# Performance work log

Measured on AMD Instinct MI355X. Metric: run time of the kernel, lower is better.

The kernel has to match this reference:

```python
import jax, jax.numpy as jnp
import numpy as np

N_NODES = 100000
NUM_GRAPHS = 128
HEADS = 4
NEG_SLOPE = 0.2  # PyG GATConv default


def _gat_conv(x, src, dst, W, att_s, att_d, bias, heads, n_nodes, concat):
    # x: [N, F_in]; W: [F_in, heads*C]; att_s/att_d: [heads, C]; bias: [heads*C] or [C]
    h = (x @ W).reshape(n_nodes, heads, -1)            # [N, H, C]
    a_s = jnp.einsum('nhc,hc->nh', h, att_s)            # [N, H]
    a_d = jnp.einsum('nhc,hc->nh', h, att_d)            # [N, H]
    e = jax.nn.leaky_relu(a_s[src] + a_d[dst], NEG_SLOPE)  # [E, H]
    m = jax.ops.segment_max(e, dst, num_segments=n_nodes)  # [N, H]
    ex = jnp.exp(e - m[dst])                                # [E, H]
    denom = jax.ops.segment_sum(ex, dst, num_segments=n_nodes)  # [N, H]
    alpha = ex / (denom[dst] + 1e-16)                       # [E, H]
    msg = h[src] * alpha[:, :, None]                        # [E, H, C]
    out = jax.ops.segment_sum(msg, dst, num_segments=n_nodes)  # [N, H, C]
    if concat:
        out = out.reshape(n_nodes, -1)                      # [N, H*C]
    else:
        out = out.mean(axis=1)                              # [N, C]
    return out + bias


def setup_inputs() -> dict:
    key = jax.random.key(0)
    ks = jax.random.split(key, 12)
    in_c, hid, out_c, H = 128, 32, 10, HEADS
    E = 1600000
    x = jax.random.normal(ks[0], (N_NODES, in_c), dtype=jnp.float32)
    edge_index = jax.random.randint(ks[1], (2, E), 0, N_NODES, dtype=jnp.int32)
    batch = jnp.sort(jax.random.randint(ks[2], (N_NODES,), 0, NUM_GRAPHS, dtype=jnp.int32))
    s1 = 1.0 / np.sqrt(in_c)
    s2 = 1.0 / np.sqrt(hid * H)
    W1 = jax.random.uniform(ks[3], (in_c, H * hid), jnp.float32, -s1, s1)
    att_src1 = jax.random.uniform(ks[4], (H, hid), jnp.float32, -s1, s1)
    att_dst1 = jax.random.uniform(ks[5], (H, hid), jnp.float32, -s1, s1)
    b1 = jnp.zeros((H * hid,), jnp.float32)
    W2 = jax.random.uniform(ks[6], (H * hid, out_c), jnp.float32, -s2, s2)
    att_src2 = jax.random.uniform(ks[7], (1, out_c), jnp.float32, -s2, s2)
    att_dst2 = jax.random.uniform(ks[8], (1, out_c), jnp.float32, -s2, s2)
    b2 = jnp.zeros((out_c,), jnp.float32)
    return {"x": x, "W1": W1, "att_src1": att_src1, "att_dst1": att_dst1, "b1": b1,
            "W2": W2, "att_src2": att_src2, "att_dst2": att_dst2, "b2": b2,
            "edge_index": edge_index, "batch": batch}


def reference(x, W1, att_src1, att_dst1, b1, W2, att_src2, att_dst2, b2, edge_index, batch):
    n = x.shape[0]
    loops = jnp.arange(n, dtype=edge_index.dtype)
    src = jnp.concatenate([edge_index[0], loops])  # add_self_loops=True
    dst = jnp.concatenate([edge_index[1], loops])
    h = jax.nn.elu(_gat_conv(x, src, dst, W1, att_src1, att_dst1, b1, HEADS, n, concat=True))
    h = jax.nn.elu(_gat_conv(h, src, dst, W2, att_src2, att_dst2, b2, 1, n, concat=False))
    # global mean pool over graphs
    sums = jax.ops.segment_sum(h, batch, num_segments=NUM_GRAPHS)
    cnts = jax.ops.segment_sum(jnp.ones((n,), h.dtype), batch, num_segments=NUM_GRAPHS)
    pooled = sums / jnp.maximum(cnts, 1.0)[:, None]
    return jax.nn.log_softmax(pooled, axis=1)
```

## Files before the change

### kernel.cpp

```cpp
#include <hip/hip_runtime.h>
#include <cstdint>
#include <cstddef>

#define LRELU(x) fmaxf((x), 0.2f*(x))

typedef float v2f __attribute__((ext_vector_type(2)));
typedef __attribute__((ext_vector_type(8))) short short8;
typedef __attribute__((ext_vector_type(4))) float f32x4;

__device__ inline unsigned short f2bf(float f) {
  unsigned u = __float_as_uint(f);
  u += 0x8000u;
  return (unsigned short)(u >> 16);
}
__device__ inline float bflo(unsigned u) { return __uint_as_float(u << 16); }
__device__ inline float bfhi(unsigned u) { return __uint_as_float(u & 0xffff0000u); }

__global__ __launch_bounds__(256) void k_gemm1(const float* __restrict__ x,
                                               const float* __restrict__ W1,
                                               const float* __restrict__ atts1,
                                               const float* __restrict__ attd1,
                                               int* __restrict__ h1f8,
                                               float* __restrict__ a_s, float* __restrict__ a_d,
                                               int* __restrict__ bcnt,
                                               float* __restrict__ poolcnt,
                                               int N) {
  __shared__ short Wt[128*136];
  int t = threadIdx.x;
  int gid = blockIdx.x*256 + t;
  if (gid < 64) bcnt[gid] = 0;
  if (gid < 1408) poolcnt[gid] = 0.f;

  {
    int n = t & 127, half = t >> 7;
    for (int kk0 = 0; kk0 < 64; kk0 += 4) {
      short v0 = (short)f2bf(W1[(half*64 + kk0 + 0)*128 + n]);
      short v1 = (short)f2bf(W1[(half*64 + kk0 + 1)*128 + n]);
      short v2 = (short)f2bf(W1[(half*64 + kk0 + 2)*128 + n]);
      short v3 = (short)f2bf(W1[(half*64 + kk0 + 3)*128 + n]);
      *(short4*)(&Wt[n*136 + half*64 + kk0]) = make_short4(v0, v1, v2, v3);
    }
  }
  __syncthreads();

  int w = t >> 6, l = t & 63;
  int n0 = blockIdx.x*64 + w*16;
  int mrow = l & 15, q = l >> 4;
  int nrow = n0 + mrow; if (nrow >= N) nrow = N - 1;
  const float4* xrow = (const float4*)(x + (size_t)nrow*128);
  f32x4 acc[8];
  #pragma unroll
  for (int i = 0; i < 8; ++i) acc[i] = (f32x4){0.f, 0.f, 0.f, 0.f};
  #pragma unroll
  for (int kc = 0; kc < 4; ++kc) {
    float4 xa = xrow[kc*8 + q*2];
    float4 xb = xrow[kc*8 + q*2 + 1];
    short8 afr;
    afr[0] = (short)f2bf(xa.x); afr[1] = (short)f2bf(xa.y);
    afr[2] = (short)f2bf(xa.z); afr[3] = (short)f2bf(xa.w);
    afr[4] = (short)f2bf(xb.x); afr[5] = (short)f2bf(xb.y);
    afr[6] = (short)f2bf(xb.z); afr[7] = (short)f2bf(xb.w);
    #pragma unroll
    for (int ti = 0; ti < 8; ++ti) {
      short8 bfr = *(const short8*)(&Wt[(ti*16 + mrow)*136 + kc*32 + q*8]);
      acc[ti] = __builtin_amdgcn_mfma_f32_16x16x32_bf16(afr, bfr, acc[ti], 0, 0, 0);
    }
  }
  __syncthreads();
  float* hs = ((float*)Wt) + w*2112;
  #pragma unroll
  for (int ti = 0; ti < 8; ++ti) {
    #pragma unroll
    for (int r = 0; r < 4; ++r)
      hs[(q*4 + r)*132 + ti*16 + mrow] = acc[ti][r];
  }
  {
    int nd = l >> 2, head = l & 3;
    int ndg = n0 + nd;
    const float4* hr  = (const float4*)(hs + nd*132 + head*32);
    const float4* asv = (const float4*)(atts1 + head*32);
    const float4* adv = (const float4*)(attd1 + head*32);
    float ps = 0.f, pd = 0.f;
    int pk[8];
    #pragma unroll
    for (int j = 0; j < 8; ++j) {
      float4 v = hr[j];
      float4 sa = asv[j], da = adv[j];
      ps += v.x*sa.x + v.y*sa.y + v.z*sa.z + v.w*sa.w;
      pd += v.x*da.x + v.y*da.y + v.z*da.z + v.w*da.w;
      int p = __builtin_amdgcn_cvt_pk_fp8_f32(v.x, v.y, 0, false);
      p = __builtin_amdgcn_cvt_pk_fp8_f32(v.z, v.w, p, true);
      pk[j] = p;
    }
    if (ndg < N) {
      int4* dst = (int4*)(h1f8 + (size_t)ndg*32 + head*8);
      dst[0] = make_int4(pk[0], pk[1], pk[2], pk[3]);
      dst[1] = make_int4(pk[4], pk[5], pk[6], pk[7]);
      a_s[ndg*4 + head] = ps;
      a_d[ndg*4 + head] = pd;
    }
  }
}

__global__ __launch_bounds__(256) void k_part(const int* __restrict__ ei, int E, int Etot,
    int Nd, int cap, int* __restrict__ bcnt, int2* __restrict__ bdata) {
  __shared__ int hist[64];
  __shared__ int cur[64];
  int t = threadIdx.x;
  if (t < 64) hist[t] = 0;
  __syncthreads();
  int base = blockIdx.x*4096;
  int dreg[16]; signed char sreg[16];
  #pragma unroll
  for (int k = 0; k < 16; ++k) {
    int e = base + k*256 + t;
    int s = -1, d = 0;
    if (e < Etot) {
      d = (e < E) ? ei[E + e] : (e - E);
      s = d / Nd;
      atomicAdd(&hist[s], 1);
    }
    dreg[k] = d; sreg[k] = (signed char)s;
  }
  __syncthreads();
  if (t < 64) cur[t] = atomicAdd(&bcnt[t], hist[t]);
  __syncthreads();
  #pragma unroll
  for (int k = 0; k < 16; ++k) {
    int s = sreg[k];
    if (s < 0) continue;
    int e = base + k*256 + t;
    int src = (e < E) ? ei[e] : dreg[k];
    int pos = atomicAdd(&cur[s], 1);
    if (pos < cap) bdata[(size_t)s*cap + pos] = make_int2(src, dreg[k]);
  }
}

__global__ __launch_bounds__(256) void k_scatter_b(const int2* __restrict__ bdata,
    const int* __restrict__ bcnt, int Nd, int cap, int N,
    int* __restrict__ deg, int* __restrict__ srcs) {
  __shared__ int lcnt[2560];
  int t = threadIdx.x;
  int s = blockIdx.x;
  int lo = s*Nd;
  for (int i = t; i < Nd; i += 256) lcnt[i] = 0;
  __syncthreads();
  int cnt = bcnt[s]; if (cnt > cap) cnt = cap;
  const int2* bp = bdata + (size_t)s*cap;
  for (int i = t; i < cnt; i += 256) {
    int2 ev = bp[i];
    int slot = atomicAdd(&lcnt[ev.y - lo], 1);
    if (slot < 64) srcs[((size_t)ev.y << 6) + slot] = ev.x;
  }
  __syncthreads();
  for (int i = t; i < Nd && lo + i < N; i += 256) deg[lo + i] = lcnt[i];
}

__global__ __launch_bounds__(256, 8) void k_agg1g2(const int* __restrict__ deg,
    const int* __restrict__ srcs, const float* __restrict__ a_s,
    const float* __restrict__ a_d, const int* __restrict__ h1f8,
    const float* __restrict__ b1, const float* __restrict__ W2,
    const float* __restrict__ atts2, const float* __restrict__ attd2,
    unsigned short* __restrict__ gb, float* __restrict__ a_s2, float* __restrict__ a_d2,
    int N) {
  __shared__ float W2t[1280];
  __shared__ float att2s[20];
  int t = threadIdx.x;
  for (int f = t; f < 1280; f += 256) {
    int c = f >> 7, k = f & 127;
    W2t[f] = W2[k*10 + c];
  }
  if (t < 20) att2s[t] = (t < 10) ? atts2[t] : attd2[t - 10];
  __syncthreads();

  int dst = (blockIdx.x*256 + t) >> 5;
  if (dst >= N) return;
  int l = t & 31;
  int sub = l & 15;
  int epair = l >> 4;
  int myhead = sub >> 2;
  int eh = l & 3;
  int ee = l >> 2;
  int beg = dst << 6;
  int dcnt = deg[dst]; if (dcnt > 64) dcnt = 64;
  int end = beg + dcnt;
  float4 ad4 = ((const float4*)a_d)[dst];
  float adh = (eh==0) ? ad4.x : (eh==1) ? ad4.y : (eh==2) ? ad4.z : ad4.w;
  float wacc = 0.f;
  v2f accA = (v2f){0.f,0.f}, accB = (v2f){0.f,0.f};
  v2f accC = (v2f){0.f,0.f}, accD = (v2f){0.f,0.f};
  const float4* as4p = (const float4*)a_s;
  const int2* h2p = (const int2*)h1f8;

  for (int g = beg; g < end; g += 32) {
    int gl = g + l;
    int se_all = srcs[gl < end ? gl : end - 1];
    int sec0 = __shfl(se_all, 0*8 + ee, 32);
    int sec1 = __shfl(se_all, 1*8 + ee, 32);
    int sec2 = __shfl(se_all, 2*8 + ee, 32);
    int sec3 = __shfl(se_all, 3*8 + ee, 32);
    float4 g0 = as4p[sec0];
    float4 g1 = as4p[sec1];
    float4 g2 = as4p[sec2];
    float4 g3 = as4p[sec3];
    float ash0 = (eh==0) ? g0.x : (eh==1) ? g0.y : (eh==2) ? g0.z : g0.w;
    float ash1 = (eh==0) ? g1.x : (eh==1) ? g1.y : (eh==2) ? g1.z : g1.w;
    float ash2 = (eh==0) ? g2.x : (eh==1) ? g2.y : (eh==2) ? g2.z : g2.w;
    float ash3 = (eh==0) ? g3.x : (eh==1) ? g3.y : (eh==2) ? g3.z : g3.w;
    float ashs[4] = {ash0, ash1, ash2, ash3};
    int nrem = end - g;
    #pragma unroll
    for (int c = 0; c < 4; ++c) {
      if (c*8 >= nrem) break;
      int rm = nrem - c*8 - 1;
      float w = __expf(LRELU(ashs[c] + adh));
      if (ee > rm) w = 0.f;
      wacc += w;
      int2 u[4]; float we[4];
      #pragma unroll
      for (int k = 0; k < 4; ++k) {
        int e = k*2 + epair;
        int s_e = __shfl(se_all, c*8 + e, 32);
        we[k]   = __shfl(w, e*4 + myhead, 32);
        u[k] = h2p[(size_t)s_e*16 + sub];
      }
      #pragma unroll
      for (int k = 0; k < 4; ++k) {
        v2f lo0 = __builtin_amdgcn_cvt_pk_f32_fp8(u[k].x, false);
        v2f hi0 = __builtin_amdgcn_cvt_pk_f32_fp8(u[k].x, true);
        v2f lo1 = __builtin_amdgcn_cvt_pk_f32_fp8(u[k].y, false);
        v2f hi1 = __builtin_amdgcn_cvt_pk_f32_fp8(u[k].y, true);
        v2f wv = (v2f){we[k], we[k]};
        accA += wv*lo0; accB += wv*hi0; accC += wv*lo1; accD += wv*hi1;
      }
    }
  }
  wacc += __shfl_xor(wacc, 4, 32);
  wacc += __shfl_xor(wacc, 8, 32);
  wacc += __shfl_xor(wacc, 16, 32);
  float denom = __shfl(wacc, myhead, 32);

  accA.x += __shfl_xor(accA.x, 16, 32); accA.y += __shfl_xor(accA.y, 16, 32);
  accB.x += __shfl_xor(accB.x, 16, 32); accB.y += __shfl_xor(accB.y, 16, 32);
  accC.x += __shfl_xor(accC.x, 16, 32); accC.y += __shfl_xor(accC.y, 16, 32);
  accD.x += __shfl_xor(accD.x, 16, 32); accD.y += __shfl_xor(accD.y, 16, 32);

  float inv = 1.0f / (denom + 1e-16f);
  float4 b1a = ((const float4*)b1)[sub*2];
  float4 b1b = ((const float4*)b1)[sub*2 + 1];
  float h0 = accA.x*inv + b1a.x; h0 = h0 > 0.f ? h0 : __expf(h0) - 1.0f;
  float h1 = accA.y*inv + b1a.y; h1 = h1 > 0.f ? h1 : __expf(h1) - 1.0f;
  float h2 = accB.x*inv + b1a.z; h2 = h2 > 0.f ? h2 : __expf(h2) - 1.0f;
  float h3 = accB.y*inv + b1a.w; h3 = h3 > 0.f ? h3 : __expf(h3) - 1.0f;
  float h4 = accC.x*inv + b1b.x; h4 = h4 > 0.f ? h4 : __expf(h4) - 1.0f;
  float h5 = accC.y*inv + b1b.y; h5 = h5 > 0.f ? h5 : __expf(h5) - 1.0f;
  float h6 = accD.x*inv + b1b.z; h6 = h6 > 0.f ? h6 : __expf(h6) - 1.0f;
  float h7 = accD.y*inv + b1b.w; h7 = h7 > 0.f ? h7 : __expf(h7) - 1.0f;

  const float4* W2t4 = (const float4*)W2t;
  float pc[5];
  #pragma unroll
  for (int cq = 0; cq < 5; ++cq) {
    int c = epair*5 + cq;
    float4 w0 = W2t4[c*32 + sub*2];
    float4 w1 = W2t4[c*32 + sub*2 + 1];
    pc[cq] = h0*w0.x + h1*w0.y + h2*w0.z + h3*w0.w
           + h4*w1.x + h5*w1.y + h6*w1.z + h7*w1.w;
  }
  #pragma unroll
  for (int off = 8; off > 0; off >>= 1) {
    #pragma unroll
    for (int cq = 0; cq < 5; ++cq)
      pc[cq] += __shfl_xor(pc[cq], off, 32);
  }
  if (sub < 5) {
    float val = pc[0];
    #pragma unroll
    for (int cq = 1; cq < 5; ++cq) val = (sub == cq) ? pc[cq] : val;
    gb[(size_t)dst*16 + epair*5 + sub] = f2bf(val);
  }
  float asH = 0.f, advH = 0.f;
  #pragma unroll
  for (int cq = 0; cq < 5; ++cq) {
    asH  += pc[cq]*att2s[epair*5 + cq];
    advH += pc[cq]*att2s[10 + epair*5 + cq];
  }
  asH  += __shfl_xor(asH, 16, 32);
  advH += __shfl_xor(advH, 16, 32);
  if (l == 0) {
    a_s2[dst] = asH;
    a_d2[dst] = advH;
  }
}

__global__ __launch_bounds__(256) void k_agg2f(const int* __restrict__ deg,
    const int* __restrict__ srcs, const float* __restrict__ a_s,
    const float* __restrict__ a_d, const unsigned short* __restrict__ gb,
    const float* __restrict__ b2, const int* __restrict__ batch,
    float* __restrict__ pooled, float* __restrict__ cnt, int N) {
  __shared__ float lp[4*10];
  __shared__ float lc[4];
  __shared__ int b0s;
  int t = threadIdx.x;
  int dst = (blockIdx.x*256 + t) >> 4;
  int l = t & 15;
  if (t < 40) lp[t] = 0.f;
  if (t < 4) lc[t] = 0.f;
  if (t == 0) {
    int d0 = (blockIdx.x*256) >> 4;
    if (d0 > N - 1) d0 = N - 1;
    b0s = batch[d0];
  }
  __syncthreads();
  int b0 = b0s;
  bool valid = (dst < N);
  float o = 0.f;
  int b = 0;
  if (valid) {
    int beg = dst << 6;
    int dcnt = deg[dst]; if (dcnt > 64) dcnt = 64;
    int end = beg + dcnt;
    float ad = a_d[dst];
    float acc[10] = {};
    float denom = 0.f;
    const uint4* g4 = (const uint4*)gb;
    const unsigned* gu = (const unsigned*)gb;
    int j = beg + l;
    if (j < end) {
      int s0 = srcs[j];
      int j1 = j + 16;
      int s1 = (j1 < end) ? srcs[j1] : s0;
      float av0 = a_s[s0];
      uint4  A0 = g4[(size_t)s0*2];
      unsigned B0 = gu[(size_t)s0*8 + 4];
      for (; j < end; j += 16) {
        float av1 = a_s[s1];
        uint4  A1 = g4[(size_t)s1*2];
        unsigned B1 = gu[(size_t)s1*8 + 4];
        int j2 = j + 32;
        int s2 = (j2 < end) ? srcs[j2] : s1;
        float w = __expf(LRELU(av0 + ad));
        denom += w;
        acc[0] += w*bflo(A0.x); acc[1] += w*bfhi(A0.x);
        acc[2] += w*bflo(A0.y); acc[3] += w*bfhi(A0.y);
        acc[4] += w*bflo(A0.z); acc[5] += w*bfhi(A0.z);
        acc[6] += w*bflo(A0.w); acc[7] += w*bfhi(A0.w);
        acc[8] += w*bflo(B0);   acc[9] += w*bfhi(B0);
        av0 = av1; A0 = A1; B0 = B1; s1 = s2;
      }
    }
    #pragma unroll
    for (int off = 8; off > 0; off >>= 1) {
      denom += __shfl_xor(denom, off, 16);
      #pragma unroll
      for (int c = 0; c < 10; ++c) acc[c] += __shfl_xor(acc[c], off, 16);
    }
    b = batch[dst];
    if (l < 10) {
      o = acc[l] / (denom + 1e-16f) + b2[l];
      o = o > 0.f ? o : __expf(o) - 1.0f;
    }
  }
  if (valid) {
    int bl = b - b0;
    if (l < 10) {
      if (bl < 4) atomicAdd(&lp[bl*10 + l], o);
      else atomicAdd(&pooled[b*10 + l], o);
    }
    if (l == 0) {
      if (bl < 4) atomicAdd(&lc[bl], 1.0f);
      else atomicAdd(&cnt[b], 1.0f);
    }
  }
  __syncthreads();
  if (t < 40) {
    int bl = t / 10, c = t - bl*10;
    int bb = b0 + bl;
    if (bb < 128 && lp[t] != 0.f) atomicAdd(&pooled[bb*10 + c], lp[t]);
  }
  if (t < 4) {
    int bb = b0 + t;
    if (bb < 128 && lc[t] != 0.f) atomicAdd(&cnt[bb], lc[t]);
  }
}

__global__ __launch_bounds__(128) void k_softmax(const float* __restrict__ pooled,
    const float* __restrict__ cnt, float* __restrict__ out) {
  int t = threadIdx.x;
  float inv = 1.0f / fmaxf(cnt[t], 1.0f);
  float v[10], m = -1e30f;
  #pragma unroll
  for (int c = 0; c < 10; ++c) { v[c] = pooled[t*10 + c] * inv; m = fmaxf(m, v[c]); }
  float s = 0.f;
  #pragma unroll
  for (int c = 0; c < 10; ++c) s += __expf(v[c] - m);
  float ls = logf(s) + m;
  #pragma unroll
  for (int c = 0; c < 10; ++c) out[t*10 + c] = v[c] - ls;
}

extern "C" void kernel_launch(void* const* d_in, const int* in_sizes, int n_in,
                              void* d_out, int out_size, void* d_ws, size_t ws_size,
                              hipStream_t stream) {
  const float* x     = (const float*)d_in[0];
  const float* W1    = (const float*)d_in[1];
  const float* atts1 = (const float*)d_in[2];
  const float* attd1 = (const float*)d_in[3];
  const float* b1    = (const float*)d_in[4];
  const float* W2    = (const float*)d_in[5];
  const float* atts2 = (const float*)d_in[6];
  const float* attd2 = (const float*)d_in[7];
  const float* b2    = (const float*)d_in[8];
  const int*   ei    = (const int*)d_in[9];
  const int*   batch = (const int*)d_in[10];
  int N = in_sizes[10];
  int E = in_sizes[9] / 2;
  int Etot = E + N;
  int Nd  = (N + 63) / 64;
  int cap = (Etot >> 6) + 4096;

  char* base = (char*)d_ws;
  size_t off = 0;
  auto allocB = [&](size_t bytes) { void* p = (void*)(base + off); off += (bytes + 63) & ~size_t(63); return p; };

  int*   h1f8   = (int*)allocB((size_t)N*32*sizeof(int));
  float* a_s1   = (float*)allocB((size_t)N*4*sizeof(float));
  float* a_d1   = (float*)allocB((size_t)N*4*sizeof(float));
  unsigned short* gb = (unsigned short*)allocB((size_t)N*16*sizeof(unsigned short));
  float* a_s2   = (float*)allocB((size_t)N*sizeof(float));
  float* a_d2   = (float*)allocB((size_t)N*sizeof(float));
  float* poolcnt= (float*)allocB(1408*sizeof(float));
  int* bcnt   = (int*)allocB(64*sizeof(int));
  int* deg    = (int*)allocB((size_t)N*sizeof(int));
  int* srcs   = (int*)allocB((size_t)N*64*sizeof(int));
  int2* bdata = (int2*)allocB((size_t)64*cap*sizeof(int2));

  float* pooled = poolcnt;
  float* cnt    = poolcnt + 1280;
  int nblkA = (Etot + 4095) / 4096;

  k_gemm1<<<dim3((N + 63)/64), dim3(256), 0, stream>>>(x, W1, atts1, attd1, h1f8,
                                                       a_s1, a_d1, bcnt, poolcnt, N);
  k_part<<<dim3(nblkA), dim3(256), 0, stream>>>(ei, E, Etot, Nd, cap, bcnt, bdata);
  k_scatter_b<<<dim3(64), dim3(256), 0, stream>>>(bdata, bcnt, Nd, cap, N, deg, srcs);
  k_agg1g2<<<dim3((N*32 + 255)/256), dim3(256), 0, stream>>>(deg, srcs, a_s1, a_d1, h1f8,
                                                             b1, W2, atts2, attd2,
                                                             gb, a_s2, a_d2, N);
  k_agg2f<<<dim3((N*16 + 255)/256), dim3(256), 0, stream>>>(deg, srcs, a_s2, a_d2, gb,
                                                            b2, batch, pooled, cnt, N);
  k_softmax<<<dim3(1), dim3(128), 0, stream>>>(pooled, cnt, (float*)d_out);
}
```

Baseline: 309.3 us.

## Fuse edge partitioning into GEMM kernel and use 256 destination buckets

Merges the edge-partition pass into the layer-1 GEMM launch by assigning extra blocks to partitioning, so the two independent stages run concurrently and one launch disappears. The bucket count goes from 64 to 256, so the scatter kernel now runs 256 blocks with smaller shared histograms, raising parallelism in that stage. The bucket counters are now cleared with a memset before the fused launch, because the GEMM blocks can no longer reset them safely. Risks are more global atomic contention spread across more buckets and a tighter per-bucket capacity margin.

```diff
diff --git a/kernel.cpp b/kernel.cpp
--- a/kernel.cpp
+++ b/kernel.cpp
@@ -16,19 +16,54 @@
 __device__ inline float bflo(unsigned u) { return __uint_as_float(u << 16); }
 __device__ inline float bfhi(unsigned u) { return __uint_as_float(u & 0xffff0000u); }
 
-__global__ __launch_bounds__(256) void k_gemm1(const float* __restrict__ x,
+__global__ __launch_bounds__(256) void k_gemm1p(const float* __restrict__ x,
                                                const float* __restrict__ W1,
                                                const float* __restrict__ atts1,
                                                const float* __restrict__ attd1,
                                                int* __restrict__ h1f8,
                                                float* __restrict__ a_s, float* __restrict__ a_d,
-                                               int* __restrict__ bcnt,
                                                float* __restrict__ poolcnt,
-                                               int N) {
+                                               int N, int gemmBlocks,
+                                               const int* __restrict__ ei, int E, int Etot,
+                                               int Nd, int cap,
+                                               int* __restrict__ bcnt, int2* __restrict__ bdata) {
   __shared__ short Wt[128*136];
   int t = threadIdx.x;
+
+  if (blockIdx.x >= gemmBlocks) {
+    int* hist = (int*)Wt;
+    int* cur  = ((int*)Wt) + 256;
+    if (t < 256) hist[t] = 0;
+    __syncthreads();
+    int base = (blockIdx.x - gemmBlocks)*4096;
+    int dreg[16]; short sreg[16];
+    #pragma unroll
+    for (int k = 0; k < 16; ++k) {
+      int e = base + k*256 + t;
+      int s = -1, d = 0;
+      if (e < Etot) {
+        d = (e < E) ? ei[E + e] : (e - E);
+        s = d / Nd;
+        atomicAdd(&hist[s], 1);
+      }
+      dreg[k] = d; sreg[k] = (short)s;
+    }
+    __syncthreads();
+    if (t < 256) cur[t] = atomicAdd(&bcnt[t], hist[t]);
+    __syncthreads();
+    #pragma unroll
+    for (int k = 0; k < 16; ++k) {
+      int s = sreg[k];
+      if (s < 0) continue;
+      int e = base + k*256 + t;
+      int src = (e < E) ? ei[e] : dreg[k];
+      int pos = atomicAdd(&cur[s], 1);
+      if (pos < cap) bdata[(size_t)s*cap + pos] = make_int2(src, dreg[k]);
+    }
+    return;
+  }
+
   int gid = blockIdx.x*256 + t;
-  if (gid < 64) bcnt[gid] = 0;
   if (gid < 1408) poolcnt[gid] = 0.f;
 
   {
@@ -102,44 +137,10 @@
   }
 }
 
-__global__ __launch_bounds__(256) void k_part(const int* __restrict__ ei, int E, int Etot,
-    int Nd, int cap, int* __restrict__ bcnt, int2* __restrict__ bdata) {
-  __shared__ int hist[64];
-  __shared__ int cur[64];
-  int t = threadIdx.x;
-  if (t < 64) hist[t] = 0;
-  __syncthreads();
-  int base = blockIdx.x*4096;
-  int dreg[16]; signed char sreg[16];
-  #pragma unroll
-  for (int k = 0; k < 16; ++k) {
-    int e = base + k*256 + t;
-    int s = -1, d = 0;
-    if (e < Etot) {
-      d = (e < E) ? ei[E + e] : (e - E);
-      s = d / Nd;
-      atomicAdd(&hist[s], 1);
-    }
-    dreg[k] = d; sreg[k] = (signed char)s;
-  }
-  __syncthreads();
-  if (t < 64) cur[t] = atomicAdd(&bcnt[t], hist[t]);
-  __syncthreads();
-  #pragma unroll
-  for (int k = 0; k < 16; ++k) {
-    int s = sreg[k];
-    if (s < 0) continue;
-    int e = base + k*256 + t;
-    int src = (e < E) ? ei[e] : dreg[k];
-    int pos = atomicAdd(&cur[s], 1);
-    if (pos < cap) bdata[(size_t)s*cap + pos] = make_int2(src, dreg[k]);
-  }
-}
-
 __global__ __launch_bounds__(256) void k_scatter_b(const int2* __restrict__ bdata,
     const int* __restrict__ bcnt, int Nd, int cap, int N,
     int* __restrict__ deg, int* __restrict__ srcs) {
-  __shared__ int lcnt[2560];
+  __shared__ int lcnt[512];
   int t = threadIdx.x;
   int s = blockIdx.x;
   int lo = s*Nd;
@@ -416,8 +417,9 @@
   int N = in_sizes[10];
   int E = in_sizes[9] / 2;
   int Etot = E + N;
-  int Nd  = (N + 63) / 64;
-  int cap = (Etot >> 6) + 4096;
+  int NB = 256;
+  int Nd  = (N + NB - 1) / NB;
+  int cap = (Etot / NB) + 2048;
 
   char* base = (char*)d_ws;
   size_t off = 0;
@@ -430,19 +432,21 @@
   float* a_s2   = (float*)allocB((size_t)N*sizeof(float));
   float* a_d2   = (float*)allocB((size_t)N*sizeof(float));
   float* poolcnt= (float*)allocB(1408*sizeof(float));
-  int* bcnt   = (int*)allocB(64*sizeof(int));
+  int* bcnt   = (int*)allocB(NB*sizeof(int));
   int* deg    = (int*)allocB((size_t)N*sizeof(int));
   int* srcs   = (int*)allocB((size_t)N*64*sizeof(int));
-  int2* bdata = (int2*)allocB((size_t)64*cap*sizeof(int2));
+  int2* bdata = (int2*)allocB((size_t)NB*cap*sizeof(int2));
 
   float* pooled = poolcnt;
   float* cnt    = poolcnt + 1280;
-  int nblkA = (Etot + 4095) / 4096;
-
-  k_gemm1<<<dim3((N + 63)/64), dim3(256), 0, stream>>>(x, W1, atts1, attd1, h1f8,
-                                                       a_s1, a_d1, bcnt, poolcnt, N);
-  k_part<<<dim3(nblkA), dim3(256), 0, stream>>>(ei, E, Etot, Nd, cap, bcnt, bdata);
-  k_scatter_b<<<dim3(64), dim3(256), 0, stream>>>(bdata, bcnt, Nd, cap, N, deg, srcs);
+  int gemmBlocks = (N + 63)/64;
+  int partBlocks = (Etot + 4095)/4096;
+
+  hipMemsetAsync(bcnt, 0, NB*sizeof(int), stream);
+  k_gemm1p<<<dim3(gemmBlocks + partBlocks), dim3(256), 0, stream>>>(
+      x, W1, atts1, attd1, h1f8, a_s1, a_d1, poolcnt, N, gemmBlocks,
+      ei, E, Etot, Nd, cap, bcnt, bdata);
+  k_scatter_b<<<dim3(NB), dim3(256), 0, stream>>>(bdata, bcnt, Nd, cap, N, deg, srcs);
   k_agg1g2<<<dim3((N*32 + 255)/256), dim3(256), 0, stream>>>(deg, srcs, a_s1, a_d1, h1f8,
                                                              b1, W2, atts2, attd2,
                                                              gb, a_s2, a_d2, N);
```

Measured after the change: 275.6 us (median of 2 runs). 1.12x faster.
